# Optimization experiments

Hardware: AMD Instinct MI355X
Metric: run time of the kernel (lower is better)

The kernel has to match this reference:

```python
import jax, jax.numpy as jnp
import numpy as np

B, S, D = 2, 2048, 1024
H, DH = 16, 64
FF = 4 * D
EPS = 1e-5
SCALE = 1.0 / np.sqrt(DH)


def setup_inputs() -> dict:
    key = jax.random.key(0)
    ks = jax.random.split(key, 8)
    std = 0.02
    return {
        "x": jax.random.normal(ks[0], (B, S, D), jnp.float32),
        "ln1_g": jnp.ones((D,), jnp.float32),
        "ln1_b": jnp.zeros((D,), jnp.float32),
        "w_qkv": jax.random.normal(ks[1], (D, 3 * H * DH), jnp.float32) * std,
        "b_qkv": jnp.zeros((3 * H * DH,), jnp.float32),
        "w_ao": jax.random.normal(ks[2], (H * DH, D), jnp.float32) * std,
        "b_ao": jnp.zeros((D,), jnp.float32),
        "ln2_g": jnp.ones((D,), jnp.float32),
        "ln2_b": jnp.zeros((D,), jnp.float32),
        "w_fc": jax.random.normal(ks[3], (D, FF), jnp.float32) * std,
        "b_fc": jnp.zeros((FF,), jnp.float32),
        "w_proj": jax.random.normal(ks[4], (FF, D), jnp.float32) * std,
        "b_proj": jnp.zeros((D,), jnp.float32),
    }


def _layernorm(x, g, b):
    mu = jnp.mean(x, axis=-1, keepdims=True)
    var = jnp.mean(jnp.square(x - mu), axis=-1, keepdims=True)
    return (x - mu) * jax.lax.rsqrt(var + EPS) * g + b


def reference(x, ln1_g, ln1_b, w_qkv, b_qkv, w_ao, b_ao,
              ln2_g, ln2_b, w_fc, b_fc, w_proj, b_proj):
    # pre-LN attention
    h = _layernorm(x, ln1_g, ln1_b)
    qkv = h @ w_qkv + b_qkv                      # [B,S,3*H*DH]
    q, k, v = jnp.split(qkv, 3, axis=-1)
    def heads(t):                                 # [B,S,H*DH] -> [B,H,S,DH]
        return t.reshape(B, S, H, DH).transpose(0, 2, 1, 3)
    q, k, v = heads(q), heads(k), heads(v)
    scores = jnp.einsum("bhsd,bhtd->bhst", q, k) * SCALE  # full [B,H,S,S]
    probs = jax.nn.softmax(scores, axis=-1)
    attn = jnp.einsum("bhst,bhtd->bhsd", probs, v)        # [B,H,S,DH]
    attn = attn.transpose(0, 2, 1, 3).reshape(B, S, H * DH)
    attn = attn @ w_ao + b_ao
    x = x + attn
    # pre-LN MLP (exact erf GELU, matches nn.GELU())
    h = _layernorm(x, ln2_g, ln2_b)
    h = jax.nn.gelu(h @ w_fc + b_fc, approximate=False)
    h = h @ w_proj + b_proj
    return x + h
```

## Files before the change

kernel.cpp:

```cpp
#include <hip/hip_runtime.h>
#include <hip/hip_bf16.h>

using short8 = __attribute__((ext_vector_type(8))) short;
using f32x4  = __attribute__((ext_vector_type(4))) float;

#define DEV __device__ __forceinline__

DEV unsigned short f2b(float f) {
  union { float f; unsigned u; } cv; cv.f = f;
  unsigned r = (cv.u + 0x7fffu + ((cv.u >> 16) & 1u)) >> 16;
  return (unsigned short)r;
}

typedef const __attribute__((address_space(1))) unsigned int* gp1;
typedef __attribute__((address_space(3))) unsigned int* lp3;
DEV void gl16(const void* g, void* l) {
  __builtin_amdgcn_global_load_lds((gp1)g, (lp3)l, 16, 0, 0);
}

__global__ void k_pre(const float* __restrict__ s0, unsigned short* __restrict__ d0,
                      const float* __restrict__ s1, unsigned short* __restrict__ d1,
                      const float* __restrict__ s2, unsigned short* __restrict__ d2,
                      const float* __restrict__ s3, unsigned short* __restrict__ d3,
                      const float* __restrict__ x, const float* __restrict__ g1,
                      const float* __restrict__ b1, unsigned short* __restrict__ y) {
  __shared__ float tile[32][33];
  __shared__ float ps[8];
  int id = blockIdx.x;
  int tx = threadIdx.x, ty = threadIdx.y;
  if (id >= 12288) {
    int row = id - 12288;
    int tid = ty * 32 + tx;
    float4 v = reinterpret_cast<const float4*>(x + (size_t)row * 1024)[tid];
    float s  = v.x + v.y + v.z + v.w;
    float s2 = v.x * v.x + v.y * v.y + v.z * v.z + v.w * v.w;
#pragma unroll
    for (int m = 1; m < 64; m <<= 1) { s += __shfl_xor(s, m); s2 += __shfl_xor(s2, m); }
    int w = tid >> 6;
    if ((tid & 63) == 0) { ps[w] = s; ps[4 + w] = s2; }
    __syncthreads();
    s  = ps[0] + ps[1] + ps[2] + ps[3];
    s2 = ps[4] + ps[5] + ps[6] + ps[7];
    float mu   = s * (1.0f / 1024.0f);
    float var  = fmaxf(s2 * (1.0f / 1024.0f) - mu * mu, 0.f);
    float rstd = rsqrtf(var + 1e-5f);
    float4 gv = reinterpret_cast<const float4*>(g1)[tid];
    float4 bv = reinterpret_cast<const float4*>(b1)[tid];
    ushort4 o;
    o.x = f2b((v.x - mu) * rstd * gv.x + bv.x);
    o.y = f2b((v.y - mu) * rstd * gv.y + bv.y);
    o.z = f2b((v.z - mu) * rstd * gv.z + bv.z);
    o.w = f2b((v.w - mu) * rstd * gv.w + bv.w);
    reinterpret_cast<ushort4*>(y + (size_t)row * 1024)[tid] = o;
    return;
  }
  const float* src; unsigned short* dst; int K, N, nx;
  if (id < 3072)      { src = s0; dst = d0; K = 1024; N = 3072; nx = 96; }
  else if (id < 4096) { id -= 3072; src = s1; dst = d1; K = 1024; N = 1024; nx = 32; }
  else if (id < 8192) { id -= 4096; src = s2; dst = d2; K = 1024; N = 4096; nx = 128; }
  else                { id -= 8192; src = s3; dst = d3; K = 4096; N = 1024; nx = 32; }
  int n0 = (id % nx) * 32, k0 = (id / nx) * 32;
#pragma unroll
  for (int j = 0; j < 4; ++j)
    tile[ty + j * 8][tx] = src[(size_t)(k0 + ty + j * 8) * N + (n0 + tx)];
  __syncthreads();
#pragma unroll
  for (int j = 0; j < 4; ++j)
    dst[(size_t)(n0 + ty + j * 8) * K + (k0 + tx)] = f2b(tile[tx][ty + j * 8]);
}

__global__ __launch_bounds__(256) void k_ln(const float* __restrict__ x,
                                            const float* __restrict__ g,
                                            const float* __restrict__ b,
                                            unsigned short* __restrict__ y) {
  int row = blockIdx.x, tid = threadIdx.x;
  float4 v = reinterpret_cast<const float4*>(x + (size_t)row * 1024)[tid];
  float s  = v.x + v.y + v.z + v.w;
  float s2 = v.x * v.x + v.y * v.y + v.z * v.z + v.w * v.w;
#pragma unroll
  for (int m = 1; m < 64; m <<= 1) { s += __shfl_xor(s, m); s2 += __shfl_xor(s2, m); }
  __shared__ float ps[8];
  int w = tid >> 6;
  if ((tid & 63) == 0) { ps[w] = s; ps[4 + w] = s2; }
  __syncthreads();
  s  = ps[0] + ps[1] + ps[2] + ps[3];
  s2 = ps[4] + ps[5] + ps[6] + ps[7];
  float mu   = s * (1.0f / 1024.0f);
  float var  = fmaxf(s2 * (1.0f / 1024.0f) - mu * mu, 0.f);
  float rstd = rsqrtf(var + 1e-5f);
  float4 gv = reinterpret_cast<const float4*>(g)[tid];
  float4 bv = reinterpret_cast<const float4*>(b)[tid];
  ushort4 o;
  o.x = f2b((v.x - mu) * rstd * gv.x + bv.x);
  o.y = f2b((v.y - mu) * rstd * gv.y + bv.y);
  o.z = f2b((v.z - mu) * rstd * gv.z + bv.z);
  o.w = f2b((v.w - mu) * rstd * gv.w + bv.w);
  reinterpret_cast<ushort4*>(y + (size_t)row * 1024)[tid] = o;
}

enum { EPI_QKV = 0, EPI_RESID = 1, EPI_GELU = 2 };

template <int EPI>
__global__ __launch_bounds__(512, 2) void k_gemm256(
    const unsigned short* __restrict__ A, const unsigned short* __restrict__ BT,
    const float* __restrict__ bias, int M, int N, int K,
    unsigned short* __restrict__ outb,
    unsigned short* __restrict__ qb, unsigned short* __restrict__ kb,
    unsigned short* __restrict__ vb) {
  __shared__ __align__(16) unsigned short Abuf[2][256][64];
  __shared__ __align__(16) unsigned short Bbuf[2][256][64];
  int nx = gridDim.x, nwg = nx * gridDim.y;
  int w0 = blockIdx.y * nx + blockIdx.x;
  int id = (w0 & 7) * (nwg >> 3) + (w0 >> 3);
  int bx = id % nx, by = id / nx;
  int m0 = by * 256, n0 = bx * 256;
  int tid = threadIdx.x;
  int lane = tid & 63, wid = tid >> 6;
  int wm = wid >> 2, wn = wid & 3;
  int l15 = lane & 15, g = lane >> 4;
  int swl = l15 & 7;
  int lrow = lane >> 3;
  int lchunk = (lane & 7) ^ lrow;
  const unsigned short* Asrc = A  + (size_t)(m0 + wid * 32 + lrow) * K + lchunk * 8;
  const unsigned short* Bsrc = BT + (size_t)(n0 + wid * 32 + lrow) * K + lchunk * 8;
  auto stage = [&](int buf, int k0) {
#pragma unroll
    for (int i = 0; i < 4; ++i)
      gl16(Asrc + k0 + (size_t)i * 8 * K, &Abuf[buf][wid * 32 + i * 8][0]);
#pragma unroll
    for (int i = 0; i < 4; ++i)
      gl16(Bsrc + k0 + (size_t)i * 8 * K, &Bbuf[buf][wid * 32 + i * 8][0]);
  };
  f32x4 acc[8][4] = {};
  int nt = K >> 6;
  stage(0, 0);
  stage(1, 64);
  asm volatile("s_waitcnt vmcnt(8)" ::: "memory");
  __builtin_amdgcn_sched_barrier(0);
  __builtin_amdgcn_s_barrier();
  int cur = 0;
  for (int t = 0; t < nt; ++t) {
    const unsigned short (*As)[64] = Abuf[cur];
    const unsigned short (*Bs)[64] = Bbuf[cur];
    short8 a0[8], b0[4], a1[8], b1[4];
#pragma unroll
    for (int mi = 0; mi < 8; ++mi)
      a0[mi] = *reinterpret_cast<const short8*>(&As[wm * 128 + mi * 16 + l15][(g ^ swl) * 8]);
#pragma unroll
    for (int ni = 0; ni < 4; ++ni)
      b0[ni] = *reinterpret_cast<const short8*>(&Bs[wn * 64 + ni * 16 + l15][(g ^ swl) * 8]);
    __builtin_amdgcn_s_setprio(1);
#pragma unroll
    for (int mi = 0; mi < 8; ++mi)
#pragma unroll
      for (int ni = 0; ni < 4; ++ni)
        acc[mi][ni] = __builtin_amdgcn_mfma_f32_16x16x32_bf16(a0[mi], b0[ni], acc[mi][ni], 0, 0, 0);
    __builtin_amdgcn_s_setprio(0);
#pragma unroll
    for (int mi = 0; mi < 8; ++mi)
      a1[mi] = *reinterpret_cast<const short8*>(&As[wm * 128 + mi * 16 + l15][((4 + g) ^ swl) * 8]);
#pragma unroll
    for (int ni = 0; ni < 4; ++ni)
      b1[ni] = *reinterpret_cast<const short8*>(&Bs[wn * 64 + ni * 16 + l15][((4 + g) ^ swl) * 8]);
    asm volatile("s_waitcnt lgkmcnt(0)" ::: "memory");
    __builtin_amdgcn_sched_barrier(0);
    __builtin_amdgcn_s_barrier();
    __builtin_amdgcn_sched_barrier(0);
    if (t + 2 < nt) stage(cur, (t + 2) << 6);
    __builtin_amdgcn_s_setprio(1);
#pragma unroll
    for (int mi = 0; mi < 8; ++mi)
#pragma unroll
      for (int ni = 0; ni < 4; ++ni)
        acc[mi][ni] = __builtin_amdgcn_mfma_f32_16x16x32_bf16(a1[mi], b1[ni], acc[mi][ni], 0, 0, 0);
    __builtin_amdgcn_s_setprio(0);
    if (t + 2 < nt) {
      asm volatile("s_waitcnt vmcnt(8)" ::: "memory");
    } else if (t + 1 < nt) {
      asm volatile("s_waitcnt vmcnt(0)" ::: "memory");
    }
    __builtin_amdgcn_sched_barrier(0);
    __builtin_amdgcn_s_barrier();
    cur ^= 1;
  }
#pragma unroll
  for (int mi = 0; mi < 8; ++mi) {
#pragma unroll
    for (int ni = 0; ni < 4; ++ni) {
      int row0 = m0 + wm * 128 + mi * 16 + g * 4;
      int col  = n0 + wn * 64 + ni * 16 + l15;
      float bcol = bias[col];
      if (EPI == EPI_QKV) {
        int which = col >> 10;
        int hc = col & 1023;
        int h = hc >> 6, d = hc & 63;
        int bb = row0 >> 11, ss0 = row0 & 2047;
        if (which == 2) {
          ushort4 pk;
          pk.x = f2b(acc[mi][ni][0] + bcol);
          pk.y = f2b(acc[mi][ni][1] + bcol);
          pk.z = f2b(acc[mi][ni][2] + bcol);
          pk.w = f2b(acc[mi][ni][3] + bcol);
          *reinterpret_cast<ushort4*>(&vb[(((size_t)(bb * 16 + h)) * 64 + d) * 2048 + ss0]) = pk;
        } else {
#pragma unroll
          for (int j = 0; j < 4; ++j) {
            float vv = acc[mi][ni][j] + bcol;
            size_t idx = (((size_t)(bb * 16 + h)) * 2048 + ss0 + j) * 64 + d;
            unsigned short bv_ = f2b(which == 0 ? vv * 0.18033688011112042f : vv);
            if (which == 0) qb[idx] = bv_;
            else            kb[idx] = bv_;
          }
        }
      } else {
#pragma unroll
        for (int j = 0; j < 4; ++j) {
          float vv = acc[mi][ni][j] + bcol;
          float ge = 0.5f * vv * (1.0f + erff(vv * 0.70710678118654752f));
          outb[(size_t)(row0 + j) * N + col] = f2b(ge);
        }
      }
    }
  }
}

__global__ __launch_bounds__(512) void k_gemm512(
    const unsigned short* __restrict__ A, const unsigned short* __restrict__ BT,
    const float* __restrict__ bias, int M, int N, int K,
    float* __restrict__ outf, const float* __restrict__ resid) {
  __shared__ __align__(16) unsigned short Abuf[2][64][64];
  __shared__ __align__(16) unsigned short Bbuf[2][128][64];
  int nx = gridDim.x, nwg = nx * gridDim.y;
  int w0 = blockIdx.y * nx + blockIdx.x;
  int id = (w0 & 7) * (nwg >> 3) + (w0 >> 3);
  int bx = id % nx, by = id / nx;
  int m0 = by * 64, n0 = bx * 128;
  int tid = threadIdx.x;
  int lane = tid & 63, wid = tid >> 6;
  int wm = wid >> 2, wn = wid & 3;
  int l15 = lane & 15, g = lane >> 4;
  int swl = l15 & 7;
  int lrow = lane >> 3;
  int lchunk = (lane & 7) ^ lrow;
  const unsigned short* Asrc = A  + (size_t)(m0 + wid * 8 + lrow) * K + lchunk * 8;
  const unsigned short* Bsrc = BT + (size_t)(n0 + wid * 16 + lrow) * K + lchunk * 8;
  auto stage = [&](int buf, int k0) {
    gl16(Asrc + k0, &Abuf[buf][wid * 8][0]);
#pragma unroll
    for (int i = 0; i < 2; ++i)
      gl16(Bsrc + k0 + (size_t)i * 8 * K, &Bbuf[buf][wid * 16 + i * 8][0]);
  };
  f32x4 acc[2][2] = {};
  int nt = K >> 6;
  stage(0, 0);
  stage(1, 64);
  asm volatile("s_waitcnt vmcnt(3)" ::: "memory");
  __builtin_amdgcn_sched_barrier(0);
  __builtin_amdgcn_s_barrier();
  int cur = 0;
  for (int t = 0; t < nt; ++t) {
    const unsigned short (*As)[64] = Abuf[cur];
    const unsigned short (*Bs)[64] = Bbuf[cur];
    short8 a0[2], b0[2], a1[2], b1[2];
#pragma unroll
    for (int mi = 0; mi < 2; ++mi)
      a0[mi] = *reinterpret_cast<const short8*>(&As[wm * 32 + mi * 16 + l15][(g ^ swl) * 8]);
#pragma unroll
    for (int ni = 0; ni < 2; ++ni)
      b0[ni] = *reinterpret_cast<const short8*>(&Bs[wn * 32 + ni * 16 + l15][(g ^ swl) * 8]);
    __builtin_amdgcn_s_setprio(1);
#pragma unroll
    for (int mi = 0; mi < 2; ++mi)
#pragma unroll
      for (int ni = 0; ni < 2; ++ni)
        acc[mi][ni] = __builtin_amdgcn_mfma_f32_16x16x32_bf16(a0[mi], b0[ni], acc[mi][ni], 0, 0, 0);
    __builtin_amdgcn_s_setprio(0);
#pragma unroll
    for (int mi = 0; mi < 2; ++mi)
      a1[mi] = *reinterpret_cast<const short8*>(&As[wm * 32 + mi * 16 + l15][((4 + g) ^ swl) * 8]);
#pragma unroll
    for (int ni = 0; ni < 2; ++ni)
      b1[ni] = *reinterpret_cast<const short8*>(&Bs[wn * 32 + ni * 16 + l15][((4 + g) ^ swl) * 8]);
    asm volatile("s_waitcnt lgkmcnt(0)" ::: "memory");
    __builtin_amdgcn_sched_barrier(0);
    __builtin_amdgcn_s_barrier();
    __builtin_amdgcn_sched_barrier(0);
    if (t + 2 < nt) stage(cur, (t + 2) << 6);
    __builtin_amdgcn_s_setprio(1);
#pragma unroll
    for (int mi = 0; mi < 2; ++mi)
#pragma unroll
      for (int ni = 0; ni < 2; ++ni)
        acc[mi][ni] = __builtin_amdgcn_mfma_f32_16x16x32_bf16(a1[mi], b1[ni], acc[mi][ni], 0, 0, 0);
    __builtin_amdgcn_s_setprio(0);
    if (t + 2 < nt) {
      asm volatile("s_waitcnt vmcnt(3)" ::: "memory");
    } else if (t + 1 < nt) {
      asm volatile("s_waitcnt vmcnt(0)" ::: "memory");
    }
    __builtin_amdgcn_sched_barrier(0);
    __builtin_amdgcn_s_barrier();
    cur ^= 1;
  }
#pragma unroll
  for (int mi = 0; mi < 2; ++mi) {
#pragma unroll
    for (int ni = 0; ni < 2; ++ni) {
      int row0 = m0 + wm * 32 + mi * 16 + g * 4;
      int col  = n0 + wn * 32 + ni * 16 + l15;
      float bcol = bias[col];
#pragma unroll
      for (int j = 0; j < 4; ++j) {
        size_t idx = (size_t)(row0 + j) * N + col;
        outf[idx] = acc[mi][ni][j] + bcol + resid[idx];
      }
    }
  }
}

__global__ __launch_bounds__(512) void k_attn(
    const unsigned short* __restrict__ qb, const unsigned short* __restrict__ kb,
    const unsigned short* __restrict__ vt, unsigned short* __restrict__ attn_out) {
  __shared__ __align__(16) unsigned short Ks[128][64];
  __shared__ __align__(16) unsigned short Vs[2][64][64];
  __shared__ __align__(16) unsigned short Plds[8][16][72];
  int bh = blockIdx.y;
  int b = bh >> 4, h = bh & 15;
  int tid = threadIdx.x;
  int lane = tid & 63, wid = tid >> 6;
  int l15 = lane & 15, g = lane >> 4;
  int q0 = blockIdx.x * 128 + wid * 16;
  const unsigned short* Qb = qb + (size_t)bh * 2048 * 64;
  const unsigned short* Kb = kb + (size_t)bh * 2048 * 64;
  const unsigned short* Vt = vt + (size_t)bh * 64 * 2048;
  short8 qf0 = *reinterpret_cast<const short8*>(&Qb[(size_t)(q0 + l15) * 64 + g * 8]);
  short8 qf1 = *reinterpret_cast<const short8*>(&Qb[(size_t)(q0 + l15) * 64 + 32 + g * 8]);
  short8 vones;
#pragma unroll
  for (int i = 0; i < 8; ++i) vones[i] = (short)0x3F80;
  float mj = 0.0f;
  f32x4 o[4] = {};
  f32x4 lacc = {};
  int kr  = wid * 16 + (lane >> 3);
  int kcn = (lane & 7) ^ (kr & 7);
  int vr  = wid * 8 + (lane >> 3);
  int vcn = (lane & 7) ^ (vr & 7);
  int swl = l15 & 7;
  for (int t0 = 0; t0 < 2048; t0 += 128) {
    __syncthreads();
    gl16(Kb + (size_t)(t0 + kr) * 64 + kcn * 8,      &Ks[wid * 16][0]);
    gl16(Kb + (size_t)(t0 + kr + 8) * 64 + kcn * 8,  &Ks[wid * 16 + 8][0]);
    gl16(Vt + (size_t)vr * 2048 + t0 + vcn * 8,      &Vs[0][wid * 8][0]);
    gl16(Vt + (size_t)vr * 2048 + t0 + 64 + vcn * 8, &Vs[1][wid * 8][0]);
    __syncthreads();
#pragma unroll
    for (int half = 0; half < 2; ++half) {
      f32x4 scv[4];
#pragma unroll
      for (int kk = 0; kk < 4; ++kk) {
        short8 kf0 = *reinterpret_cast<const short8*>(&Ks[half * 64 + kk * 16 + l15][(g ^ swl) * 8]);
        short8 kf1 = *reinterpret_cast<const short8*>(&Ks[half * 64 + kk * 16 + l15][((4 + g) ^ swl) * 8]);
        f32x4 z = {};
        z = __builtin_amdgcn_mfma_f32_16x16x32_bf16(kf0, qf0, z, 0, 0, 0);
        scv[kk] = __builtin_amdgcn_mfma_f32_16x16x32_bf16(kf1, qf1, z, 0, 0, 0);
      }
      float p[16];
#pragma unroll
      for (int kk = 0; kk < 4; ++kk)
#pragma unroll
        for (int j = 0; j < 4; ++j)
          p[kk * 4 + j] = __builtin_amdgcn_exp2f(scv[kk][j] - mj);
#pragma unroll
      for (int kk = 0; kk < 4; ++kk) {
        unsigned r0, r1;
        asm("v_cvt_pk_bf16_f32 %0, %1, %2" : "=v"(r0) : "v"(p[kk * 4 + 0]), "v"(p[kk * 4 + 1]));
        asm("v_cvt_pk_bf16_f32 %0, %1, %2" : "=v"(r1) : "v"(p[kk * 4 + 2]), "v"(p[kk * 4 + 3]));
        unsigned long long w = (unsigned long long)r0 | ((unsigned long long)r1 << 32);
        *reinterpret_cast<unsigned long long*>(&Plds[wid][l15][kk * 16 + g * 4]) = w;
      }
      float t0m = fmaxf(fmaxf(scv[0][0], scv[0][1]), fmaxf(scv[0][2], scv[0][3]));
      float t1m = fmaxf(fmaxf(scv[1][0], scv[1][1]), fmaxf(scv[1][2], scv[1][3]));
      float t2m = fmaxf(fmaxf(scv[2][0], scv[2][1]), fmaxf(scv[2][2], scv[2][3]));
      float t3m = fmaxf(fmaxf(scv[3][0], scv[3][1]), fmaxf(scv[3][2], scv[3][3]));
      float mx = fmaxf(fmaxf(t0m, t1m), fmaxf(t2m, t3m));
      mx = fmaxf(mx, __shfl_xor(mx, 16));
      mx = fmaxf(mx, __shfl_xor(mx, 32));
      if (!__all(mx <= mj + 8.0f)) {
        float mnew = fmaxf(mj, mx);
        float ef = __builtin_amdgcn_exp2f(mj - mnew);
        int sb = 20 * g;
        float e0 = __shfl(ef, sb + 0), e1 = __shfl(ef, sb + 1);
        float e2 = __shfl(ef, sb + 2), e3 = __shfl(ef, sb + 3);
#pragma unroll
        for (int ct = 0; ct < 4; ++ct) {
          o[ct][0] *= e0; o[ct][1] *= e1; o[ct][2] *= e2; o[ct][3] *= e3;
        }
        lacc[0] *= e0; lacc[1] *= e1; lacc[2] *= e2; lacc[3] *= e3;
#pragma unroll
        for (int kk = 0; kk < 4; ++kk) {
#pragma unroll
          for (int j = 0; j < 4; ++j)
            p[kk * 4 + j] = __builtin_amdgcn_exp2f(scv[kk][j] - mnew);
          unsigned r0, r1;
          asm("v_cvt_pk_bf16_f32 %0, %1, %2" : "=v"(r0) : "v"(p[kk * 4 + 0]), "v"(p[kk * 4 + 1]));
          asm("v_cvt_pk_bf16_f32 %0, %1, %2" : "=v"(r1) : "v"(p[kk * 4 + 2]), "v"(p[kk * 4 + 3]));
          unsigned long long w = (unsigned long long)r0 | ((unsigned long long)r1 << 32);
          *reinterpret_cast<unsigned long long*>(&Plds[wid][l15][kk * 16 + g * 4]) = w;
        }
        mj = mnew;
      }
      short8 pf0 = *reinterpret_cast<const short8*>(&Plds[wid][l15][g * 8]);
      short8 pf1 = *reinterpret_cast<const short8*>(&Plds[wid][l15][32 + g * 8]);
      lacc = __builtin_amdgcn_mfma_f32_16x16x32_bf16(pf0, vones, lacc, 0, 0, 0);
      lacc = __builtin_amdgcn_mfma_f32_16x16x32_bf16(pf1, vones, lacc, 0, 0, 0);
#pragma unroll
      for (int ct = 0; ct < 4; ++ct) {
        short8 vf0 = *reinterpret_cast<const short8*>(&Vs[half][ct * 16 + l15][(g ^ swl) * 8]);
        short8 vf1 = *reinterpret_cast<const short8*>(&Vs[half][ct * 16 + l15][((4 + g) ^ swl) * 8]);
        o[ct] = __builtin_amdgcn_mfma_f32_16x16x32_bf16(pf0, vf0, o[ct], 0, 0, 0);
        o[ct] = __builtin_amdgcn_mfma_f32_16x16x32_bf16(pf1, vf1, o[ct], 0, 0, 0);
      }
    }
  }
#pragma unroll
  for (int j = 0; j < 4; ++j) {
    float iv = 1.0f / lacc[j];
    size_t t = (size_t)b * 2048 + (q0 + g * 4 + j);
#pragma unroll
    for (int ct = 0; ct < 4; ++ct)
      attn_out[t * 1024 + h * 64 + ct * 16 + l15] = f2b(o[ct][j] * iv);
  }
}

extern "C" void kernel_launch(void* const* d_in, const int* in_sizes, int n_in,
                              void* d_out, int out_size, void* d_ws, size_t ws_size,
                              hipStream_t stream) {
  (void)in_sizes; (void)n_in; (void)out_size; (void)ws_size;
  const float* x      = (const float*)d_in[0];
  const float* ln1_g  = (const float*)d_in[1];
  const float* ln1_b  = (const float*)d_in[2];
  const float* w_qkv  = (const float*)d_in[3];
  const float* b_qkv  = (const float*)d_in[4];
  const float* w_ao   = (const float*)d_in[5];
  const float* b_ao   = (const float*)d_in[6];
  const float* ln2_g  = (const float*)d_in[7];
  const float* ln2_b  = (const float*)d_in[8];
  const float* w_fc   = (const float*)d_in[9];
  const float* b_fc   = (const float*)d_in[10];
  const float* w_proj = (const float*)d_in[11];
  const float* b_proj = (const float*)d_in[12];
  float* out = (float*)d_out;

  char* ws = (char*)d_ws;
  size_t o = 0;
  auto nxt = [&](size_t bytes) { void* p = ws + o; o += (bytes + 255) & ~(size_t)255; return p; };
  unsigned short* wT_qkv  = (unsigned short*)nxt((size_t)3072 * 1024 * 2);
  unsigned short* wT_ao   = (unsigned short*)nxt((size_t)1024 * 1024 * 2);
  unsigned short* wT_fc   = (unsigned short*)nxt((size_t)4096 * 1024 * 2);
  unsigned short* wT_proj = (unsigned short*)nxt((size_t)1024 * 4096 * 2);
  unsigned short* h_ln    = (unsigned short*)nxt((size_t)4096 * 1024 * 2);
  unsigned short* qbuf    = (unsigned short*)nxt((size_t)4096 * 1024 * 2);
  unsigned short* kbuf    = (unsigned short*)nxt((size_t)4096 * 1024 * 2);
  unsigned short* vtb     = (unsigned short*)nxt((size_t)4096 * 1024 * 2);
  unsigned short* attn_o  = (unsigned short*)nxt((size_t)4096 * 1024 * 2);
  float*          out1    = (float*)nxt((size_t)4096 * 1024 * 4);
  unsigned short* fc_buf  = qbuf;

  dim3 b32(32, 8, 1);
  k_pre<<<16384, b32, 0, stream>>>(w_qkv, wT_qkv, w_ao, wT_ao, w_fc, wT_fc, w_proj, wT_proj,
                                   x, ln1_g, ln1_b, h_ln);
  k_gemm256<EPI_QKV><<<dim3(12, 16), 512, 0, stream>>>(h_ln, wT_qkv, b_qkv, 4096, 3072, 1024,
                                                       nullptr, qbuf, kbuf, vtb);
  k_attn<<<dim3(16, 32), 512, 0, stream>>>(qbuf, kbuf, vtb, attn_o);
  k_gemm512<<<dim3(8, 64), 512, 0, stream>>>(attn_o, wT_ao, b_ao, 4096, 1024, 1024,
                                             out1, x);
  k_ln<<<4096, 256, 0, stream>>>(out1, ln2_g, ln2_b, h_ln);
  k_gemm256<EPI_GELU><<<dim3(16, 16), 512, 0, stream>>>(h_ln, wT_fc, b_fc, 4096, 4096, 1024,
                                                        fc_buf, nullptr, nullptr, nullptr);
  k_gemm512<<<dim3(8, 64), 512, 0, stream>>>(fc_buf, wT_proj, b_proj, 4096, 1024, 4096,
                                             out, out1);
}
```

Measured before the change: 225.0 us.

## Split attention KV range in two and merge partials in a combine kernel

The attention grid grows from 512 to 1024 blocks, with each block covering half of the key/value sequence. Each block writes an unnormalized bf16 partial output plus its row sum and running max. A new combine kernel rescales the two partials by exp2 of their max differences and normalizes them. This is meant to raise occupancy across the GPU's compute units, at the cost of extra global traffic, a second launch, and an additional bf16 rounding of the partials.

After: 232.5 us. +3.3%, slower.

```diff
diff --git a/kernel.cpp b/kernel.cpp
--- a/kernel.cpp
+++ b/kernel.cpp
@@ -10,6 +10,9 @@
   union { float f; unsigned u; } cv; cv.f = f;
   unsigned r = (cv.u + 0x7fffu + ((cv.u >> 16) & 1u)) >> 16;
   return (unsigned short)r;
+}
+DEV float b2f(unsigned short u) {
+  union { unsigned u; float f; } cv; cv.u = ((unsigned)u) << 16; return cv.f;
 }
 
 typedef const __attribute__((address_space(1))) unsigned int* gp1;
@@ -320,7 +323,9 @@
 
 __global__ __launch_bounds__(512) void k_attn(
     const unsigned short* __restrict__ qb, const unsigned short* __restrict__ kb,
-    const unsigned short* __restrict__ vt, unsigned short* __restrict__ attn_out) {
+    const unsigned short* __restrict__ vt,
+    unsigned short* __restrict__ op0, unsigned short* __restrict__ op1,
+    float* __restrict__ lbuf, float* __restrict__ mbuf) {
   __shared__ __align__(16) unsigned short Ks[128][64];
   __shared__ __align__(16) unsigned short Vs[2][64][64];
   __shared__ __align__(16) unsigned short Plds[8][16][72];
@@ -329,7 +334,8 @@
   int tid = threadIdx.x;
   int lane = tid & 63, wid = tid >> 6;
   int l15 = lane & 15, g = lane >> 4;
-  int q0 = blockIdx.x * 128 + wid * 16;
+  int qblk = blockIdx.x & 15, sp = blockIdx.x >> 4;
+  int q0 = qblk * 128 + wid * 16;
   const unsigned short* Qb = qb + (size_t)bh * 2048 * 64;
   const unsigned short* Kb = kb + (size_t)bh * 2048 * 64;
   const unsigned short* Vt = vt + (size_t)bh * 64 * 2048;
@@ -346,7 +352,8 @@
   int vr  = wid * 8 + (lane >> 3);
   int vcn = (lane & 7) ^ (vr & 7);
   int swl = l15 & 7;
-  for (int t0 = 0; t0 < 2048; t0 += 128) {
+  int tbeg = sp << 10, tend = tbeg + 1024;
+  for (int t0 = tbeg; t0 < tend; t0 += 128) {
     __syncthreads();
     gl16(Kb + (size_t)(t0 + kr) * 64 + kcn * 8,      &Ks[wid * 16][0]);
     gl16(Kb + (size_t)(t0 + kr + 8) * 64 + kcn * 8,  &Ks[wid * 16 + 8][0]);
@@ -422,14 +429,42 @@
       }
     }
   }
+  unsigned short* op = sp ? op1 : op0;
 #pragma unroll
   for (int j = 0; j < 4; ++j) {
-    float iv = 1.0f / lacc[j];
-    size_t t = (size_t)b * 2048 + (q0 + g * 4 + j);
+    int s = q0 + g * 4 + j;
+    size_t t = (size_t)b * 2048 + s;
 #pragma unroll
     for (int ct = 0; ct < 4; ++ct)
-      attn_out[t * 1024 + h * 64 + ct * 16 + l15] = f2b(o[ct][j] * iv);
-  }
+      op[t * 1024 + h * 64 + ct * 16 + l15] = f2b(o[ct][j]);
+    if (l15 == 0) {
+      lbuf[((size_t)sp * 4096 + t) * 16 + h] = lacc[j];
+      mbuf[((size_t)sp * 4096 + t) * 16 + h] = mj;
+    }
+  }
+}
+
+__global__ __launch_bounds__(256) void k_comb(
+    unsigned short* __restrict__ op0, const unsigned short* __restrict__ op1,
+    const float* __restrict__ lbuf, const float* __restrict__ mbuf) {
+  size_t bs = blockIdx.x;
+  int tid = threadIdx.x;
+  int c0 = tid * 4;
+  int h = c0 >> 6;
+  float l0 = lbuf[bs * 16 + h], m0 = mbuf[bs * 16 + h];
+  float l1 = lbuf[(4096 + bs) * 16 + h], m1 = mbuf[(4096 + bs) * 16 + h];
+  float M = fmaxf(m0, m1);
+  float s0 = __builtin_amdgcn_exp2f(m0 - M);
+  float s1 = __builtin_amdgcn_exp2f(m1 - M);
+  float inv = 1.0f / (l0 * s0 + l1 * s1);
+  ushort4 a0 = *reinterpret_cast<const ushort4*>(&op0[bs * 1024 + c0]);
+  ushort4 a1 = *reinterpret_cast<const ushort4*>(&op1[bs * 1024 + c0]);
+  ushort4 r;
+  r.x = f2b((b2f(a0.x) * s0 + b2f(a1.x) * s1) * inv);
+  r.y = f2b((b2f(a0.y) * s0 + b2f(a1.y) * s1) * inv);
+  r.z = f2b((b2f(a0.z) * s0 + b2f(a1.z) * s1) * inv);
+  r.w = f2b((b2f(a0.w) * s0 + b2f(a1.w) * s1) * inv);
+  *reinterpret_cast<ushort4*>(&op0[bs * 1024 + c0]) = r;
 }
 
 extern "C" void kernel_launch(void* const* d_in, const int* in_sizes, int n_in,
@@ -465,13 +500,17 @@
   unsigned short* attn_o  = (unsigned short*)nxt((size_t)4096 * 1024 * 2);
   float*          out1    = (float*)nxt((size_t)4096 * 1024 * 4);
   unsigned short* fc_buf  = qbuf;
+  unsigned short* op1  = (unsigned short*)out1;
+  float*          lbuf = (float*)((char*)out1 + (size_t)4096 * 1024 * 2);
+  float*          mbuf = (float*)((char*)out1 + (size_t)4096 * 1024 * 2 + (size_t)2 * 4096 * 16 * 4);
 
   dim3 b32(32, 8, 1);
   k_pre<<<16384, b32, 0, stream>>>(w_qkv, wT_qkv, w_ao, wT_ao, w_fc, wT_fc, w_proj, wT_proj,
                                    x, ln1_g, ln1_b, h_ln);
   k_gemm256<EPI_QKV><<<dim3(12, 16), 512, 0, stream>>>(h_ln, wT_qkv, b_qkv, 4096, 3072, 1024,
                                                        nullptr, qbuf, kbuf, vtb);
-  k_attn<<<dim3(16, 32), 512, 0, stream>>>(qbuf, kbuf, vtb, attn_o);
+  k_attn<<<dim3(32, 32), 512, 0, stream>>>(qbuf, kbuf, vtb, attn_o, op1, lbuf, mbuf);
+  k_comb<<<4096, 256, 0, stream>>>(attn_o, op1, lbuf, mbuf);
   k_gemm512<<<dim3(8, 64), 512, 0, stream>>>(attn_o, wT_ao, b_ao, 4096, 1024, 1024,
                                              out1, x);
   k_ln<<<4096, 256, 0, stream>>>(out1, ln2_g, ln2_b, h_ln);
```
